# Kernel optimization log

Measured on AMD Instinct MI355X. Metric: run time of the kernel, lower is better.

Reference implementation:

```python
import jax, jax.numpy as jnp
import numpy as np

EMB = 1024
HID = 2048
HEADS = 16
CONV = 4


def causal_conv1d(z, w):
    # z: [B, H, T], w: [H, K] depthwise causal conv
    K = w.shape[1]
    T = z.shape[-1]
    zp = jnp.pad(z, ((0, 0), (0, 0), (K - 1, 0)))  # [B, H, T+K-1]
    out = jnp.zeros_like(z)
    for k in range(K):  # tiny fixed loop over taps (K<=4)
        out = out + w[None, :, k, None] * jax.lax.dynamic_slice_in_dim(zp, k, T, axis=2)
    return out


def linear_scan(a, b):
    # h_t = a_t * h_{t-1} + b_t along last axis; associative scan
    def combine(c1, c2):
        a1, b1 = c1
        a2, b2 = c2
        return a1 * a2, a2 * b1 + b2
    _, h = jax.lax.associative_scan(combine, (a, b), axis=-1)
    return h


def setup_inputs() -> dict:
    key = jax.random.key(0)
    k1, k2, k3, k4 = jax.random.split(key, 4)
    x = jax.random.normal(k1, (4, 2048, EMB), dtype=jnp.float32)
    w1 = jax.random.normal(k2, (3 * HID, EMB), dtype=jnp.float32) * (EMB ** -0.5)
    w2 = jax.random.normal(k3, (EMB, HID), dtype=jnp.float32) * (HID ** -0.5)
    conv_weight = jax.random.normal(k4, (HID, CONV), dtype=jnp.float32) * (CONV ** -0.5)
    return {"x": x, "w1": w1, "w2": w2, "conv_weight": conv_weight}


def reference(x, w1, w2, conv_weight):
    bsz, seq_len, _ = x.shape
    head_dim = HID // HEADS
    y = jnp.einsum("bse,he->bsh", x, w1)  # [B, S, 3*HID]
    out1, z, h = jnp.split(y, 3, axis=-1)
    z = jnp.swapaxes(z, 1, 2)  # [B, HID, S]
    h = jnp.swapaxes(h, 1, 2)
    z = causal_conv1d(z, conv_weight)
    z = jax.nn.sigmoid(z)
    z = z.reshape(bsz * HEADS, head_dim, seq_len)
    h = h.reshape(bsz * HEADS, head_dim, seq_len)
    h = linear_scan(1.0 - z, z * h)
    out2 = jnp.swapaxes(h.reshape(bsz, HID, seq_len), 1, 2)  # [B, S, HID]
    out = jax.nn.silu(out1) * out2
    return jnp.einsum("bsh,eh->bse", out, w2)
```

## Files before the change

kernel.cpp:

```cpp
#include <hip/hip_runtime.h>
#include <cstdint>

#define EMB 1024
#define HID 2048
#define BATCH 4
#define SEQ 2048
#define MROWS (BATCH * SEQ)
#define N1 (3 * HID)
#define K1 EMB
#define N2 EMB
#define K2 HID

#define NX (MROWS * EMB)
#define NW1 (N1 * K1)
#define NW2 (N2 * K2)

#define SEG 32
#define SLEN (SEQ / SEG)

typedef unsigned short ushort_t;
typedef __bf16 bf16x8 __attribute__((ext_vector_type(8)));
typedef float f32x4 __attribute__((ext_vector_type(4)));
typedef ushort_t us4 __attribute__((ext_vector_type(4)));

__device__ __forceinline__ ushort_t f2bf(float f) {
    uint32_t u = __builtin_bit_cast(uint32_t, f);
    u += 0x7fffu + ((u >> 16) & 1u);
    return (ushort_t)(u >> 16);
}
__device__ __forceinline__ float bf2f(ushort_t h) {
    uint32_t u = ((uint32_t)h) << 16;
    return __builtin_bit_cast(float, u);
}
__device__ __forceinline__ float bflo(uint32_t v) {
    return __builtin_bit_cast(float, v << 16);
}
__device__ __forceinline__ float bfhi(uint32_t v) {
    return __builtin_bit_cast(float, v & 0xffff0000u);
}
__device__ __forceinline__ float sigm(float x) {
    return 1.f / (1.f + __expf(-x));
}

__device__ __forceinline__ void gload_lds16(const ushort_t* g, const ushort_t* l) {
    __builtin_amdgcn_global_load_lds(
        (const __attribute__((address_space(1))) void*)(uintptr_t)(g),
        (__attribute__((address_space(3))) void*)(uint32_t)(uintptr_t)(l),
        16, 0, 0);
}

__global__ __launch_bounds__(256) void cvt_kernel(
    const float* __restrict__ x, const float* __restrict__ w1,
    const float* __restrict__ w2, ushort_t* __restrict__ xb,
    ushort_t* __restrict__ w1b, ushort_t* __restrict__ w2b) {
    const int i = (blockIdx.x * 256 + threadIdx.x) * 4;
    const float* s;
    ushort_t* d;
    if (i < NX) {
        s = x + i; d = xb + i;
    } else if (i < NX + NW1) {
        s = w1 + (i - NX); d = w1b + (i - NX);
    } else {
        s = w2 + (i - NX - NW1); d = w2b + (i - NX - NW1);
    }
    const float4 v = *(const float4*)s;
    us4 o;
    o.x = f2bf(v.x); o.y = f2bf(v.y); o.z = f2bf(v.z); o.w = f2bf(v.w);
    *(us4*)d = o;
}

template <bool OUT_BF16>
__global__ __launch_bounds__(256) void gemm_bt(
    const ushort_t* __restrict__ A, const ushort_t* __restrict__ B,
    void* __restrict__ Cv, int M, int N, int K) {
    __shared__ ushort_t sA[2 * 128 * 32];
    __shared__ ushort_t sB[2 * 128 * 32];

    const int tid  = threadIdx.x;
    const int lane = tid & 63;
    const int wave = tid >> 6;
    const int quad = lane >> 4;
    const int l16  = lane & 15;
    const long tm0 = (long)blockIdx.y * 128;
    const long tn0 = (long)blockIdx.x * 128;
    const int wm = (wave & 1) * 64;
    const int wn = (wave >> 1) * 64;

    f32x4 acc[4][4] = {};

    const int ar0 = tid >> 2;
    const int ar1 = (tid + 256) >> 2;
    const int kq  = (tid & 3) ^ ((ar0 >> 1) & 3);
    const int ac  = kq * 8;
    const ushort_t* gA = A + (size_t)tm0 * K;
    const ushort_t* gB = B + (size_t)tn0 * K;

    const int rsw = (l16 >> 1) & 3;
    const int aoff = (quad ^ rsw) * 8 + l16 * 32;

    for (int k0 = 0; k0 < K; k0 += 64) {
        __syncthreads();
#pragma unroll
        for (int p = 0; p < 2; ++p) {
            const int kp = k0 + p * 32;
            ushort_t* pA = &sA[p * 4096];
            ushort_t* pB = &sB[p * 4096];
            gload_lds16(gA + (size_t)ar0 * K + kp + ac, pA + wave * 512);
            gload_lds16(gA + (size_t)ar1 * K + kp + ac, pA + 2048 + wave * 512);
            gload_lds16(gB + (size_t)ar0 * K + kp + ac, pB + wave * 512);
            gload_lds16(gB + (size_t)ar1 * K + kp + ac, pB + 2048 + wave * 512);
        }
        __syncthreads();

#pragma unroll
        for (int p = 0; p < 2; ++p) {
            const ushort_t* pA = &sA[p * 4096];
            const ushort_t* pB = &sB[p * 4096];
            bf16x8 af[4], bfr[4];
#pragma unroll
            for (int i = 0; i < 4; ++i)
                af[i] = *(const bf16x8*)&pA[(wm + i * 16) * 32 + aoff];
#pragma unroll
            for (int j = 0; j < 4; ++j)
                bfr[j] = *(const bf16x8*)&pB[(wn + j * 16) * 32 + aoff];
#pragma unroll
            for (int i = 0; i < 4; ++i)
#pragma unroll
                for (int j = 0; j < 4; ++j)
                    acc[i][j] = __builtin_amdgcn_mfma_f32_16x16x32_bf16(
                        af[i], bfr[j], acc[i][j], 0, 0, 0);
        }
    }

#pragma unroll
    for (int i = 0; i < 4; ++i) {
        const long row0 = tm0 + wm + i * 16 + quad * 4;
#pragma unroll
        for (int j = 0; j < 4; ++j) {
            const long col = tn0 + wn + j * 16 + l16;
#pragma unroll
            for (int r = 0; r < 4; ++r) {
                if constexpr (OUT_BF16) {
                    ((ushort_t*)Cv)[(size_t)(row0 + r) * N + col] = f2bf(acc[i][j][r]);
                } else {
                    ((float*)Cv)[(size_t)(row0 + r) * N + col] = acc[i][j][r];
                }
            }
        }
    }
}

__global__ __launch_bounds__(256) void scan_part1(
    const ushort_t* __restrict__ y, const float* __restrict__ cw,
    float* __restrict__ Ag, float* __restrict__ Bg) {
    const int gid = blockIdx.x * 256 + threadIdx.x;
    const int ch  = (gid & 1023) * 2;
    const int bs  = gid >> 10;
    const int b   = bs >> 5;
    const int seg = bs & 31;
    const int t0  = seg * SLEN;
    const size_t rowbase = (size_t)b * SEQ;
    const ushort_t* yz = y + 2048 + ch;
    const ushort_t* yh = y + 4096 + ch;

    float w[2][4];
#pragma unroll
    for (int c = 0; c < 2; ++c)
#pragma unroll
        for (int k = 0; k < 4; ++k) w[c][k] = cw[(ch + c) * 4 + k];

    auto ld2 = [&](const ushort_t* p, int t) -> uint32_t {
        return *(const uint32_t*)(p + (rowbase + (size_t)t) * 6144);
    };
    auto zpair = [&](int t, float* out) {
        if (t < 0) { out[0] = 0.f; out[1] = 0.f; }
        else { uint32_t v = ld2(yz, t); out[0] = bflo(v); out[1] = bfhi(v); }
    };

    float z1[2], z2[2], z3[2], A[2] = {1.f, 1.f}, Bv[2] = {0.f, 0.f};
    zpair(t0 - 1, z1); zpair(t0 - 2, z2); zpair(t0 - 3, z3);

#pragma unroll 4
    for (int t = t0; t < t0 + SLEN; ++t) {
        const uint32_t vz = ld2(yz, t);
        const uint32_t vh = ld2(yh, t);
        const float zr[2] = {bflo(vz), bfhi(vz)};
        const float hr[2] = {bflo(vh), bfhi(vh)};
#pragma unroll
        for (int c = 0; c < 2; ++c) {
            const float cv = w[c][0] * z3[c] + w[c][1] * z2[c] +
                             w[c][2] * z1[c] + w[c][3] * zr[c];
            const float s = sigm(cv);
            z3[c] = z2[c]; z2[c] = z1[c]; z1[c] = zr[c];
            const float a = 1.f - s;
            A[c] *= a;
            Bv[c] = a * Bv[c] + s * hr[c];
        }
    }
    const size_t idx = ((size_t)b * SEG + seg) * HID + ch;
    *(float2*)&Ag[idx] = make_float2(A[0], A[1]);
    *(float2*)&Bg[idx] = make_float2(Bv[0], Bv[1]);
}

__global__ __launch_bounds__(256) void scan_part2(
    const float* __restrict__ Ag, const float* __restrict__ Bg,
    float* __restrict__ Cr) {
    const int gid = blockIdx.x * 256 + threadIdx.x;
    const int b  = gid >> 11;
    const int ch = gid & 2047;
    float carry = 0.f;
#pragma unroll
    for (int s = 0; s < SEG; ++s) {
        const size_t idx = ((size_t)b * SEG + s) * HID + ch;
        Cr[idx] = carry;
        carry = Ag[idx] * carry + Bg[idx];
    }
}

__global__ __launch_bounds__(256) void scan_part3(
    const ushort_t* __restrict__ y, const float* __restrict__ cw,
    const float* __restrict__ Cr, ushort_t* __restrict__ u) {
    const int gid = blockIdx.x * 256 + threadIdx.x;
    const int ch  = (gid & 1023) * 2;
    const int bs  = gid >> 10;
    const int b   = bs >> 5;
    const int seg = bs & 31;
    const int t0  = seg * SLEN;
    const size_t rowbase = (size_t)b * SEQ;
    const ushort_t* yo = y + ch;
    const ushort_t* yz = y + 2048 + ch;
    const ushort_t* yh = y + 4096 + ch;

    float w[2][4];
#pragma unroll
    for (int c = 0; c < 2; ++c)
#pragma unroll
        for (int k = 0; k < 4; ++k) w[c][k] = cw[(ch + c) * 4 + k];

    auto ld2 = [&](const ushort_t* p, int t) -> uint32_t {
        return *(const uint32_t*)(p + (rowbase + (size_t)t) * 6144);
    };
    auto zpair = [&](int t, float* out) {
        if (t < 0) { out[0] = 0.f; out[1] = 0.f; }
        else { uint32_t v = ld2(yz, t); out[0] = bflo(v); out[1] = bfhi(v); }
    };

    const size_t cidx = ((size_t)b * SEG + seg) * HID + ch;
    float h[2] = {Cr[cidx], Cr[cidx + 1]};
    float z1[2], z2[2], z3[2];
    zpair(t0 - 1, z1); zpair(t0 - 2, z2); zpair(t0 - 3, z3);

#pragma unroll 4
    for (int t = t0; t < t0 + SLEN; ++t) {
        const uint32_t vz = ld2(yz, t);
        const uint32_t vh = ld2(yh, t);
        const uint32_t vo = ld2(yo, t);
        const float zr[2] = {bflo(vz), bfhi(vz)};
        const float hr[2] = {bflo(vh), bfhi(vh)};
        const float o1[2] = {bflo(vo), bfhi(vo)};
        ushort_t res[2];
#pragma unroll
        for (int c = 0; c < 2; ++c) {
            const float cv = w[c][0] * z3[c] + w[c][1] * z2[c] +
                             w[c][2] * z1[c] + w[c][3] * zr[c];
            const float s = sigm(cv);
            z3[c] = z2[c]; z2[c] = z1[c]; z1[c] = zr[c];
            h[c] = (1.f - s) * h[c] + s * hr[c];
            const float sil = o1[c] * sigm(o1[c]);
            res[c] = f2bf(sil * h[c]);
        }
        *(uint32_t*)&u[(rowbase + (size_t)t) * (size_t)HID + ch] =
            (uint32_t)res[0] | ((uint32_t)res[1] << 16);
    }
}

extern "C" void kernel_launch(void* const* d_in, const int* in_sizes, int n_in,
                              void* d_out, int out_size, void* d_ws, size_t ws_size,
                              hipStream_t stream) {
    const float* x  = (const float*)d_in[0];
    const float* w1 = (const float*)d_in[1];
    const float* w2 = (const float*)d_in[2];
    const float* cw = (const float*)d_in[3];
    char* ws = (char*)d_ws;

    ushort_t* xb  = (ushort_t*)(ws);
    ushort_t* w1b = (ushort_t*)(ws + (size_t)16777216);
    ushort_t* w2b = (ushort_t*)(ws + (size_t)29360128);
    ushort_t* y   = (ushort_t*)(ws + (size_t)33554432);
    ushort_t* u   = (ushort_t*)(ws + (size_t)134217728);
    float* Ag = (float*)(ws);
    float* Bg = (float*)(ws + (size_t)1048576);
    float* Cr = (float*)(ws + (size_t)2097152);
    float* out = (float*)d_out;

    cvt_kernel<<<16384, 256, 0, stream>>>(x, w1, w2, xb, w1b, w2b);
    gemm_bt<true><<<dim3(N1 / 128, MROWS / 128), 256, 0, stream>>>(
        xb, w1b, (void*)y, MROWS, N1, K1);
    scan_part1<<<512, 256, 0, stream>>>(y, cw, Ag, Bg);
    scan_part2<<<32, 256, 0, stream>>>(Ag, Bg, Cr);
    scan_part3<<<512, 256, 0, stream>>>(y, cw, Cr, u);
    gemm_bt<false><<<dim3(N2 / 128, MROWS / 128), 256, 0, stream>>>(
        u, w2b, (void*)out, MROWS, N2, K2);
}
```

Measured before the change: 324.4 us.

## Replace first GEMM with 256x256-tile 8-wave pipelined MFMA kernel

Adds a new GEMM kernel using 256x256 output tiles, 512 threads, double-buffered LDS filled by direct global-to-LDS loads, and a four-phase ping-pong schedule with barriers and priority raising around the MFMA blocks. It also remaps workgroup ids for XCD locality. It is used only for the large first projection GEMM, to raise data reuse per loaded byte and overlap loads with compute. The cost is 128KB of LDS, many accumulator registers, and hand-tuned waitcnt counts that must be exactly right.

```diff
diff --git a/kernel.cpp b/kernel.cpp
--- a/kernel.cpp
+++ b/kernel.cpp
@@ -150,6 +150,171 @@
     }
 }
 
+__device__ __forceinline__ void lda4(bf16x8 (&af)[2][4], const ushort_t* c,
+                                     int arow, int quad, int sw) {
+#pragma unroll
+    for (int s = 0; s < 2; ++s)
+#pragma unroll
+        for (int i = 0; i < 4; ++i)
+            af[s][i] = *(const bf16x8*)&c[(arow + i * 16) * 64 +
+                                          (((s * 4 + quad) ^ sw) << 3)];
+}
+__device__ __forceinline__ void ldb2(bf16x8 (&bfr)[2][2], const ushort_t* c,
+                                     int bcol, int quad, int sw) {
+#pragma unroll
+    for (int s = 0; s < 2; ++s)
+#pragma unroll
+        for (int j = 0; j < 2; ++j)
+            bfr[s][j] = *(const bf16x8*)&c[(bcol + j * 16) * 64 +
+                                           (((s * 4 + quad) ^ sw) << 3)];
+}
+template <int QM, int QN>
+__device__ __forceinline__ void mm16(f32x4 (&acc)[8][4],
+                                     const bf16x8 (&af)[2][4],
+                                     const bf16x8 (&bfr)[2][2]) {
+#pragma unroll
+    for (int s = 0; s < 2; ++s)
+#pragma unroll
+        for (int i = 0; i < 4; ++i)
+#pragma unroll
+            for (int j = 0; j < 2; ++j)
+                acc[QM * 4 + i][QN * 2 + j] =
+                    __builtin_amdgcn_mfma_f32_16x16x32_bf16(
+                        af[s][i], bfr[s][j], acc[QM * 4 + i][QN * 2 + j], 0, 0, 0);
+}
+
+template <bool OUT_BF16>
+__global__ __launch_bounds__(512, 2) void gemm256(
+    const ushort_t* __restrict__ A, const ushort_t* __restrict__ B,
+    void* __restrict__ Cv, int M, int N, int K) {
+    __shared__ __align__(16) ushort_t sA[2][2][8192];
+    __shared__ __align__(16) ushort_t sB[2][2][8192];
+
+    const int tid  = threadIdx.x;
+    const int lane = tid & 63;
+    const int wave = tid >> 6;
+    const int wm   = wave >> 2;
+    const int wn   = wave & 3;
+    const int quad = lane >> 4;
+    const int l15  = lane & 15;
+    const int sw   = lane & 7;
+
+    int wg = blockIdx.x;
+    const int nwg = gridDim.x;
+    if ((nwg & 7) == 0) wg = (wg & 7) * (nwg >> 3) + (wg >> 3);
+    const int nbx = N >> 8;
+    const int bx = wg % nbx;
+    const int by = wg / nbx;
+    const long tm0 = (long)by << 8;
+    const long tn0 = (long)bx << 8;
+
+    const ushort_t* gA = A + (size_t)tm0 * K;
+    const ushort_t* gB = B + (size_t)tn0 * K;
+
+    const int l8 = lane >> 3;
+    const int ss = (lane & 7) ^ l8;
+    const uint32_t rA = (uint32_t)((wave & 3) * 16 + l8 + (wave >> 2) * 128);
+    const int cB = wave * 16 + l8;
+    const uint32_t rB = (uint32_t)((cB >> 5) * 64 + (cB & 31));
+    const uint32_t offA0 = rA * (uint32_t)K + (uint32_t)ss * 8u;
+    const uint32_t offA1 = offA0 + 8u * (uint32_t)K;
+    const uint32_t offB0 = rB * (uint32_t)K + (uint32_t)ss * 8u;
+    const uint32_t offB1 = offB0 + 8u * (uint32_t)K;
+
+    const auto stA = [&](int tt, int q) {
+        ushort_t* d = &sA[tt & 1][q][wave << 10];
+        const size_t ko = (size_t)tt * 64 + (size_t)q * 64 * (size_t)K;
+        gload_lds16(gA + ko + offA0, d);
+        gload_lds16(gA + ko + offA1, d + 512);
+    };
+    const auto stB = [&](int tt, int q) {
+        ushort_t* d = &sB[tt & 1][q][wave << 10];
+        const size_t ko = (size_t)tt * 64 + (size_t)q * 32 * (size_t)K;
+        gload_lds16(gB + ko + offB0, d);
+        gload_lds16(gB + ko + offB1, d + 512);
+    };
+
+    const int arow = wm * 64 + l15;
+    const int bcol = wn * 32 + l15;
+
+    f32x4 acc[8][4] = {};
+    bf16x8 af[2][4], bfr[2][2];
+
+    const int NT = K >> 6;
+
+    stA(0, 0); stB(0, 0); stB(0, 1); stA(0, 1);
+    stA(1, 0); stB(1, 1); stA(1, 1);
+    asm volatile("s_waitcnt vmcnt(6)" ::: "memory");
+    __builtin_amdgcn_s_barrier();
+
+    for (int T = 0; T < NT; ++T) {
+        const int cur = T & 1;
+        const ushort_t* a0 = &sA[cur][0][0];
+        const ushort_t* a1 = &sA[cur][1][0];
+        const ushort_t* b0 = &sB[cur][0][0];
+        const ushort_t* b1 = &sB[cur][1][0];
+        const bool st1 = (T + 1 < NT);
+        const bool st2 = (T + 2 < NT);
+
+        lda4(af, a0, arow, quad, sw);
+        ldb2(bfr, b0, bcol, quad, sw);
+        if (st1) stB(T + 1, 0);
+        asm volatile("s_waitcnt lgkmcnt(8)" ::: "memory");
+        __builtin_amdgcn_s_barrier();
+        asm volatile("s_waitcnt lgkmcnt(0)" ::: "memory");
+        __builtin_amdgcn_s_setprio(1);
+        mm16<0, 0>(acc, af, bfr);
+        __builtin_amdgcn_s_setprio(0);
+        __builtin_amdgcn_s_barrier();
+
+        ldb2(bfr, b1, bcol, quad, sw);
+        if (st2) stA(T + 2, 0);
+        __builtin_amdgcn_s_barrier();
+        asm volatile("s_waitcnt lgkmcnt(0)" ::: "memory");
+        __builtin_amdgcn_s_setprio(1);
+        mm16<0, 1>(acc, af, bfr);
+        __builtin_amdgcn_s_setprio(0);
+        __builtin_amdgcn_s_barrier();
+
+        lda4(af, a1, arow, quad, sw);
+        if (st2) stB(T + 2, 1);
+        __builtin_amdgcn_s_barrier();
+        asm volatile("s_waitcnt lgkmcnt(0)" ::: "memory");
+        __builtin_amdgcn_s_setprio(1);
+        mm16<1, 1>(acc, af, bfr);
+        __builtin_amdgcn_s_setprio(0);
+        __builtin_amdgcn_s_barrier();
+
+        ldb2(bfr, b0, bcol, quad, sw);
+        if (st2) stA(T + 2, 1);
+        __builtin_amdgcn_s_barrier();
+        asm volatile("s_waitcnt lgkmcnt(0)" ::: "memory");
+        __builtin_amdgcn_s_setprio(1);
+        mm16<1, 0>(acc, af, bfr);
+        __builtin_amdgcn_s_setprio(0);
+        if (st2)      asm volatile("s_waitcnt vmcnt(6)" ::: "memory");
+        else if (st1) asm volatile("s_waitcnt vmcnt(0)" ::: "memory");
+        __builtin_amdgcn_s_barrier();
+    }
+
+#pragma unroll
+    for (int ai = 0; ai < 8; ++ai) {
+        const long row0 = tm0 + wm * 128 + (ai >> 2) * 64 + (ai & 3) * 16 + quad * 4;
+#pragma unroll
+        for (int bj = 0; bj < 4; ++bj) {
+            const long col = tn0 + wn * 64 + (bj >> 1) * 32 + (bj & 1) * 16 + l15;
+#pragma unroll
+            for (int r = 0; r < 4; ++r) {
+                if constexpr (OUT_BF16) {
+                    ((ushort_t*)Cv)[(size_t)(row0 + r) * N + col] = f2bf(acc[ai][bj][r]);
+                } else {
+                    ((float*)Cv)[(size_t)(row0 + r) * N + col] = acc[ai][bj][r];
+                }
+            }
+        }
+    }
+}
+
 __global__ __launch_bounds__(256) void scan_part1(
     const ushort_t* __restrict__ y, const float* __restrict__ cw,
     float* __restrict__ Ag, float* __restrict__ Bg) {
@@ -294,8 +459,7 @@
     float* out = (float*)d_out;
 
     cvt_kernel<<<16384, 256, 0, stream>>>(x, w1, w2, xb, w1b, w2b);
-    gemm_bt<true><<<dim3(N1 / 128, MROWS / 128), 256, 0, stream>>>(
-        xb, w1b, (void*)y, MROWS, N1, K1);
+    gemm256<true><<<dim3(768), 512, 0, stream>>>(xb, w1b, (void*)y, MROWS, N1, K1);
     scan_part1<<<512, 256, 0, stream>>>(y, cw, Ag, Bg);
     scan_part2<<<32, 256, 0, stream>>>(Ag, Bg, Cr);
     scan_part3<<<512, 256, 0, stream>>>(y, cw, Cr, u);
```

After: 325.4 us. About the same (+0.3%).
